# Kernel tuning notes

Hardware: AMD Instinct MI355X
Metric: run time of the kernel (lower is better)

## Reference

```python
import jax, jax.numpy as jnp
import numpy as np

D_MODEL = 1024
H = 16
D_K = D_MODEL // H
B = 4
S = 2048
NEG = -1.0e9


def setup_inputs() -> dict:
    key = jax.random.key(0)
    ks = jax.random.split(key, 12)
    scale = 1.0 / np.sqrt(D_MODEL)
    inp = {
        "q": jax.random.normal(ks[0], (B, S, D_MODEL), jnp.float32),
        "k": jax.random.normal(ks[1], (B, S, D_MODEL), jnp.float32),
        "v": jax.random.normal(ks[2], (B, S, D_MODEL), jnp.float32),
        "mask": jax.random.randint(ks[3], (1, 1, S, S), 0, 2, jnp.int32),
        # nn.Linear params: y = x @ W.T + b
        "Wq": jax.random.normal(ks[4], (D_MODEL, D_MODEL), jnp.float32) * scale,
        "bq": jnp.zeros((D_MODEL,), jnp.float32),
        "Wk": jax.random.normal(ks[5], (D_MODEL, D_MODEL), jnp.float32) * scale,
        "bk": jnp.zeros((D_MODEL,), jnp.float32),
        "Wv": jax.random.normal(ks[6], (D_MODEL, D_MODEL), jnp.float32) * scale,
        "bv": jnp.zeros((D_MODEL,), jnp.float32),
        "Wo": jax.random.normal(ks[7], (D_MODEL, D_MODEL), jnp.float32) * scale,
        "bo": jnp.zeros((D_MODEL,), jnp.float32),
    }
    return inp


def reference(q, k, v, mask, Wq, bq, Wk, bk, Wv, bv, Wo, bo):
    # QKV projections (torch Linear: x @ W.T + b)
    query = q @ Wq.T + bq                       # [B,S,D]
    key_ = k @ Wk.T + bk
    value = v @ Wv.T + bv
    # [B,S,D] -> [B,H,S,d_k]
    def split_heads(x):
        return x.reshape(B, S, H, D_K).transpose(0, 2, 1, 3)
    query, key_, value = split_heads(query), split_heads(key_), split_heads(value)
    # scaled dot-product attention
    scores = jnp.einsum("bhqd,bhkd->bhqk", query, key_) / np.sqrt(D_K)
    scores = jnp.where(mask == 0, NEG, scores)  # masked_fill(mask==0, -1e9)
    attn = jax.nn.softmax(scores, axis=-1)      # dropout p=0 -> identity
    x = jnp.einsum("bhqk,bhkd->bhqd", attn, value)
    # merge heads and output projection
    x = x.transpose(0, 2, 1, 3).reshape(B, S, D_MODEL)
    return x @ Wo.T + bo
```

## Files before the change

kernel.cpp:

```cpp
#include <hip/hip_runtime.h>
#include <hip/hip_bf16.h>

typedef __bf16 bf16;
typedef __bf16 bf16x8 __attribute__((ext_vector_type(8)));
typedef __bf16 bf16x4 __attribute__((ext_vector_type(4)));
typedef float  f32x4v __attribute__((ext_vector_type(4)));

#define MFMA16(a, b, c) __builtin_amdgcn_mfma_f32_16x16x32_bf16((a), (b), (c), 0, 0, 0)

static constexpr int D_MODEL = 1024;
static constexpr int NH      = 16;
static constexpr int DK      = 64;
static constexpr int BATCH   = 4;
static constexpr int SEQ     = 2048;

__device__ __forceinline__ void glds16(const void* g, void* l) {
    __builtin_amdgcn_global_load_lds((const __attribute__((address_space(1))) void*)g,
                                     (__attribute__((address_space(3))) void*)l, 16, 0, 0);
}

struct CvtArgs {
    const float* s[7];
    bf16* d[7];
    int n[7];
};

__global__ __launch_bounds__(256) void cvt7(CvtArgs a) {
    const int which = blockIdx.y;
    const int i = (blockIdx.x * 256 + threadIdx.x) * 8;
    if (i >= a.n[which]) return;
    const float4 v0 = *(const float4*)(a.s[which] + i);
    const float4 v1 = *(const float4*)(a.s[which] + i + 4);
    bf16x8 o = {(bf16)v0.x, (bf16)v0.y, (bf16)v0.z, (bf16)v0.w,
                (bf16)v1.x, (bf16)v1.y, (bf16)v1.z, (bf16)v1.w};
    *(bf16x8*)(a.d[which] + i) = o;
}

__global__ __launch_bounds__(256) void mask_prep(const int* __restrict__ m,
                                                 bf16* __restrict__ Mr) {
    const int o = blockIdx.x * 256 + threadIdx.x;
    const int row = o >> 11, j = o & 2047;
    const int g = j >> 6, idx = j & 63;
    const int incol = (g << 6) + (((idx >> 2) & 3) << 4) + ((idx >> 4) << 2) + (idx & 3);
    Mr[o] = m[row * 2048 + incol] ? (bf16)0.0f : (bf16)-16384.0f;
}

template <int MODE>
__global__ __launch_bounds__(256) void gemm_bt(const bf16* __restrict__ A,
                                               const bf16* __restrict__ W,
                                               const float* __restrict__ bias,
                                               void* __restrict__ outv) {
    __shared__ bf16 Als[128 * 32];
    __shared__ bf16 Bls[128 * 32];

    const int tid  = threadIdx.x;
    const int wave = tid >> 6;
    const int lane = tid & 63;
    const int l15  = lane & 15;
    const int quad = lane >> 4;
    const int L    = blockIdx.x;
    const int m0   = ((L & 7) | ((L >> 6) << 3)) * 128;
    const int n0   = ((L >> 3) & 7) * 128;
    const int wm   = (wave >> 1) * 64;
    const int wn   = (wave & 1) * 64;

    f32x4v acc[4][4];
#pragma unroll
    for (int i = 0; i < 4; ++i)
#pragma unroll
        for (int j = 0; j < 4; ++j) acc[i][j] = (f32x4v){0.f, 0.f, 0.f, 0.f};

    const int r_a    = wave * 16 + (lane >> 2);
    const int c_a    = (lane & 3) * 8;
    const int ldsoff = wave * 512;

    for (int k0 = 0; k0 < 1024; k0 += 32) {
        __syncthreads();
#pragma unroll
        for (int p = 0; p < 2; ++p) {
            const int row = p * 64 + r_a;
            glds16(A + (size_t)(m0 + row) * 1024 + k0 + c_a, &Als[p * 2048 + ldsoff]);
            glds16(W + (size_t)(n0 + row) * 1024 + k0 + c_a, &Bls[p * 2048 + ldsoff]);
        }
        __syncthreads();

        bf16x8 af[4], bfr[4];
#pragma unroll
        for (int i = 0; i < 4; ++i)
            af[i] = *(const bf16x8*)(&Als[(wm + i * 16 + l15) * 32 + quad * 8]);
#pragma unroll
        for (int j = 0; j < 4; ++j)
            bfr[j] = *(const bf16x8*)(&Bls[(wn + j * 16 + l15) * 32 + quad * 8]);
#pragma unroll
        for (int i = 0; i < 4; ++i)
#pragma unroll
            for (int j = 0; j < 4; ++j) acc[i][j] = MFMA16(af[i], bfr[j], acc[i][j]);
    }

#pragma unroll
    for (int j = 0; j < 4; ++j) {
        const int col = n0 + wn + j * 16 + l15;
        const float bs = bias[col];
        const int h = col >> 6, dk = col & 63;
        if (MODE == 1) {
            bf16* out = (bf16*)outv;
            const int sg = m0 + wm;
            const int bb = sg >> 11, sb = sg & 2047;
            const size_t rowbase = ((size_t)((bb * NH + h) * 64 + dk)) * SEQ + sb;
#pragma unroll
            for (int i = 0; i < 4; ++i) {
                bf16x4 v = {(bf16)(acc[i][j][0] + bs), (bf16)(acc[i][j][1] + bs),
                            (bf16)(acc[i][j][2] + bs), (bf16)(acc[i][j][3] + bs)};
                *(bf16x4*)(&out[rowbase + quad * 16 + i * 4]) = v;
            }
        } else {
#pragma unroll
            for (int i = 0; i < 4; ++i) {
                const int r4 = m0 + wm + i * 16 + quad * 4;
                const int b = r4 >> 11, sb = r4 & 2047;
                if (MODE == 2) {
                    float* out = (float*)outv;
#pragma unroll
                    for (int reg = 0; reg < 4; ++reg)
                        out[(size_t)(r4 + reg) * 1024 + col] = acc[i][j][reg] + bs;
                } else {
                    bf16* out = (bf16*)outv;
#pragma unroll
                    for (int reg = 0; reg < 4; ++reg)
                        out[((size_t)(b * NH + h) * SEQ + sb + reg) * 64 + dk] =
                            (bf16)(acc[i][j][reg] + bs);
                }
            }
        }
    }
}

__global__ __launch_bounds__(256, 2) void attn_kernel(const bf16* __restrict__ Qh,
                                                      const bf16* __restrict__ Kh,
                                                      const bf16* __restrict__ Vtg,
                                                      const bf16* __restrict__ Mr,
                                                      bf16* __restrict__ Xout) {
    __shared__ bf16 Kls[4096];
    __shared__ bf16 Vls[4096];

    const int tid  = threadIdx.x;
    const int wave = tid >> 6;
    const int lane = tid & 63;
    const int l15  = lane & 15;
    const int quad = lane >> 4;
    const int bh   = blockIdx.x;
    const int q0   = blockIdx.y * 256;

    const size_t base = (size_t)bh * SEQ * DK;
    const bf16* Q  = Qh + base;
    const bf16* K  = Kh + base;
    const bf16* Vg = Vtg + base;

    const int qw = q0 + wave * 64;
    bf16x8 aq[4][2];
#pragma unroll
    for (int rb = 0; rb < 4; ++rb)
#pragma unroll
        for (int kk = 0; kk < 2; ++kk)
            aq[rb][kk] = *(const bf16x8*)(Q + (size_t)(qw + rb * 16 + l15) * 64 +
                                          kk * 32 + quad * 8);

    bf16x8 ones;
#pragma unroll
    for (int t = 0; t < 8; ++t) ones[t] = (bf16)1.0f;

    f32x4v acc[4][4];
    f32x4v sacc[4];
#pragma unroll
    for (int rb = 0; rb < 4; ++rb) {
        sacc[rb] = (f32x4v){0.f, 0.f, 0.f, 0.f};
#pragma unroll
        for (int x = 0; x < 4; ++x) acc[rb][x] = (f32x4v){0.f, 0.f, 0.f, 0.f};
    }

    constexpr float CLOG = 0.125f * 1.4426950408889634f;
    const bf16* mbase = Mr + (size_t)(qw + l15) * 2048 + quad * 16;

    for (int kt = 0; kt < SEQ; kt += 64) {
        __syncthreads();
#pragma unroll
        for (int p = 0; p < 2; ++p) {
            const int kc = wave * 2 + p;
            glds16(K + (size_t)(kt + lane) * 64 + kc * 8, &Kls[kc * 512]);
            glds16(Vg + (size_t)lane * SEQ + kt + kc * 8, &Vls[kc * 512]);
        }
        bf16x8 mv[4][2];
#pragma unroll
        for (int rb = 0; rb < 4; ++rb)
#pragma unroll
            for (int h2 = 0; h2 < 2; ++h2)
                mv[rb][h2] = *(const bf16x8*)(mbase + (size_t)(rb * 16) * 2048 +
                                              kt + h2 * 8);
        __syncthreads();

        bf16x8 ak[4][2];
#pragma unroll
        for (int n16 = 0; n16 < 4; ++n16)
#pragma unroll
            for (int kk = 0; kk < 2; ++kk)
                ak[n16][kk] = *(const bf16x8*)(&Kls[((kk * 4 + quad) * 64 + n16 * 16 + l15) * 8]);

        bf16x8 pa[4][2];
#pragma unroll
        for (int rb = 0; rb < 4; ++rb) {
            f32x4v sv[4];
            __builtin_amdgcn_s_setprio(1);
#pragma unroll
            for (int n16 = 0; n16 < 4; ++n16) {
                f32x4v t = (f32x4v){0.f, 0.f, 0.f, 0.f};
                t = MFMA16(ak[n16][0], aq[rb][0], t);
                t = MFMA16(ak[n16][1], aq[rb][1], t);
                sv[n16] = t;
            }
            __builtin_amdgcn_s_setprio(0);
#pragma unroll
            for (int n16 = 0; n16 < 4; ++n16)
#pragma unroll
                for (int reg = 0; reg < 4; ++reg) {
                    const float e = exp2f(fmaf(sv[n16][reg], CLOG,
                                               (float)mv[rb][n16 >> 1][(n16 & 1) * 4 + reg]));
                    pa[rb][n16 >> 1][(n16 & 1) * 4 + reg] = (bf16)e;
                }
        }

        __builtin_amdgcn_s_setprio(1);
#pragma unroll
        for (int rb = 0; rb < 4; ++rb) {
            sacc[rb] = MFMA16(pa[rb][0], ones, sacc[rb]);
            sacc[rb] = MFMA16(pa[rb][1], ones, sacc[rb]);
        }
#pragma unroll
        for (int nt = 0; nt < 4; ++nt) {
            const bf16x8 bv0 = *(const bf16x8*)(&Vls[((quad * 2 + 0) * 64 + nt * 16 + l15) * 8]);
            const bf16x8 bv1 = *(const bf16x8*)(&Vls[((quad * 2 + 1) * 64 + nt * 16 + l15) * 8]);
#pragma unroll
            for (int rb = 0; rb < 4; ++rb) {
                acc[rb][nt] = MFMA16(pa[rb][0], bv0, acc[rb][nt]);
                acc[rb][nt] = MFMA16(pa[rb][1], bv1, acc[rb][nt]);
            }
        }
        __builtin_amdgcn_s_setprio(0);
    }

    const int b = bh >> 4, h = bh & 15;
#pragma unroll
    for (int rb = 0; rb < 4; ++rb) {
        float rinv[4];
#pragma unroll
        for (int reg = 0; reg < 4; ++reg) rinv[reg] = 1.0f / sacc[rb][reg];
#pragma unroll
        for (int nt = 0; nt < 4; ++nt)
#pragma unroll
            for (int reg = 0; reg < 4; ++reg) {
                const int sg = qw + rb * 16 + quad * 4 + reg;
                Xout[(size_t)(b * SEQ + sg) * D_MODEL + h * 64 + nt * 16 + l15] =
                    (bf16)(acc[rb][nt][reg] * rinv[reg]);
            }
    }
}

extern "C" void kernel_launch(void* const* d_in, const int* in_sizes, int n_in,
                              void* d_out, int out_size, void* d_ws, size_t ws_size,
                              hipStream_t stream) {
    const float* q    = (const float*)d_in[0];
    const float* k    = (const float*)d_in[1];
    const float* v    = (const float*)d_in[2];
    const int*   mask = (const int*)d_in[3];
    const float* Wq   = (const float*)d_in[4];
    const float* bq   = (const float*)d_in[5];
    const float* Wk   = (const float*)d_in[6];
    const float* bk   = (const float*)d_in[7];
    const float* Wv   = (const float*)d_in[8];
    const float* bv   = (const float*)d_in[9];
    const float* Wo   = (const float*)d_in[10];
    const float* bo   = (const float*)d_in[11];

    const size_t T = (size_t)BATCH * SEQ * D_MODEL;
    const size_t WN = (size_t)D_MODEL * D_MODEL;
    char* w = (char*)d_ws;
    bf16* Qh  = (bf16*)w;            w += T * 2;
    bf16* Kh  = (bf16*)w;            w += T * 2;
    bf16* Vt  = (bf16*)w;            w += T * 2;
    bf16* Mr  = (bf16*)w;            w += (size_t)SEQ * SEQ * 2;
    bf16* qb  = (bf16*)w;            w += T * 2;
    bf16* kb  = (bf16*)w;            w += T * 2;
    bf16* vb  = (bf16*)w;            w += T * 2;
    bf16* Wqb = (bf16*)w;            w += WN * 2;
    bf16* Wkb = (bf16*)w;            w += WN * 2;
    bf16* Wvb = (bf16*)w;            w += WN * 2;
    bf16* Wob = (bf16*)w;            w += WN * 2;

    CvtArgs ca;
    ca.s[0] = q;  ca.d[0] = qb;  ca.n[0] = (int)T;
    ca.s[1] = k;  ca.d[1] = kb;  ca.n[1] = (int)T;
    ca.s[2] = v;  ca.d[2] = vb;  ca.n[2] = (int)T;
    ca.s[3] = Wq; ca.d[3] = Wqb; ca.n[3] = (int)WN;
    ca.s[4] = Wk; ca.d[4] = Wkb; ca.n[4] = (int)WN;
    ca.s[5] = Wv; ca.d[5] = Wvb; ca.n[5] = (int)WN;
    ca.s[6] = Wo; ca.d[6] = Wob; ca.n[6] = (int)WN;

    cvt7<<<dim3(4096, 7), 256, 0, stream>>>(ca);
    mask_prep<<<dim3((SEQ * SEQ) / 256), 256, 0, stream>>>(mask, Mr);

    dim3 gg(512);
    gemm_bt<0><<<gg, 256, 0, stream>>>(qb, Wqb, bq, (void*)Qh);
    gemm_bt<0><<<gg, 256, 0, stream>>>(kb, Wkb, bk, (void*)Kh);
    gemm_bt<1><<<gg, 256, 0, stream>>>(vb, Wvb, bv, (void*)Vt);

    attn_kernel<<<dim3(BATCH * NH, SEQ / 256), 256, 0, stream>>>(Qh, Kh, Vt, Mr, qb);

    gemm_bt<2><<<gg, 256, 0, stream>>>(qb, Wob, bo, d_out);
}
```

Baseline: 391.7 us.

## Fuse prep launches, batch QKV GEMMs, double-buffer attention K/V, fold scale into Q

The mask preprocessing is merged into the conversion kernel, which now handles 8 elements per thread, and the three QKV projection GEMMs run as one launch with a 3D grid. The softmax scale is folded into the Q projection, and the mask bias seeds the score accumulator, so the exp path needs no fma. Attention K/V tiles are double-buffered in LDS, prefetching the next tile while the current one is computed, with one barrier per iteration. This cuts launch overhead and load-latency stalls, but doubles attention LDS use, which may affect occupancy at 2 blocks per CU.

New measurement: 395.0 us. Within noise of the previous version (+0.8%).

```diff
diff --git a/kernel.cpp b/kernel.cpp
--- a/kernel.cpp
+++ b/kernel.cpp
@@ -13,6 +13,7 @@
 static constexpr int DK      = 64;
 static constexpr int BATCH   = 4;
 static constexpr int SEQ     = 2048;
+static constexpr float CLOG  = 0.125f * 1.4426950408889634f;
 
 __device__ __forceinline__ void glds16(const void* g, void* l) {
     __builtin_amdgcn_global_load_lds((const __attribute__((address_space(1))) void*)g,
@@ -23,11 +24,28 @@
     const float* s[7];
     bf16* d[7];
     int n[7];
+    const int* mask;
+    bf16* Mr;
 };
 
-__global__ __launch_bounds__(256) void cvt7(CvtArgs a) {
+__global__ __launch_bounds__(256) void cvt8(CvtArgs a) {
     const int which = blockIdx.y;
     const int i = (blockIdx.x * 256 + threadIdx.x) * 8;
+    if (which == 7) {
+        if (i >= SEQ * SEQ) return;
+        const int row = i >> 11, j0 = i & 2047;
+        const int g = j0 >> 6;
+        bf16x8 o;
+#pragma unroll
+        for (int t = 0; t < 8; ++t) {
+            const int idx = (j0 + t) & 63;
+            const int incol =
+                (g << 6) + (((idx >> 2) & 3) << 4) + ((idx >> 4) << 2) + (idx & 3);
+            o[t] = a.mask[row * 2048 + incol] ? (bf16)0.0f : (bf16)-16384.0f;
+        }
+        *(bf16x8*)(a.Mr + i) = o;
+        return;
+    }
     if (i >= a.n[which]) return;
     const float4 v0 = *(const float4*)(a.s[which] + i);
     const float4 v1 = *(const float4*)(a.s[which] + i + 4);
@@ -36,22 +54,22 @@
     *(bf16x8*)(a.d[which] + i) = o;
 }
 
-__global__ __launch_bounds__(256) void mask_prep(const int* __restrict__ m,
-                                                 bf16* __restrict__ Mr) {
-    const int o = blockIdx.x * 256 + threadIdx.x;
-    const int row = o >> 11, j = o & 2047;
-    const int g = j >> 6, idx = j & 63;
-    const int incol = (g << 6) + (((idx >> 2) & 3) << 4) + ((idx >> 4) << 2) + (idx & 3);
-    Mr[o] = m[row * 2048 + incol] ? (bf16)0.0f : (bf16)-16384.0f;
-}
-
-template <int MODE>
-__global__ __launch_bounds__(256) void gemm_bt(const bf16* __restrict__ A,
-                                               const bf16* __restrict__ W,
-                                               const float* __restrict__ bias,
-                                               void* __restrict__ outv) {
+struct G3 {
+    const bf16* A[3];
+    const bf16* W[3];
+    const float* bias[3];
+    bf16* out[3];
+};
+
+__global__ __launch_bounds__(256) void gemm_qkv(G3 g) {
     __shared__ bf16 Als[128 * 32];
     __shared__ bf16 Bls[128 * 32];
+
+    const int which = blockIdx.y;
+    const bf16* __restrict__ A   = g.A[which];
+    const bf16* __restrict__ W   = g.W[which];
+    const float* __restrict__ bias = g.bias[which];
+    const float scale = (which == 0) ? CLOG : 1.0f;
 
     const int tid  = threadIdx.x;
     const int wave = tid >> 6;
@@ -97,40 +115,97 @@
             for (int j = 0; j < 4; ++j) acc[i][j] = MFMA16(af[i], bfr[j], acc[i][j]);
     }
 
+    bf16* out = g.out[which];
+#pragma unroll
+    for (int j = 0; j < 4; ++j) {
+        const int col = n0 + wn + j * 16 + l15;
+        const float bs_s = bias[col] * scale;
+        const int h = col >> 6, dk = col & 63;
+        if (which == 2) {
+            const int sg = m0 + wm;
+            const int bb = sg >> 11, sb = sg & 2047;
+            const size_t rowbase = ((size_t)((bb * NH + h) * 64 + dk)) * SEQ + sb;
+#pragma unroll
+            for (int i = 0; i < 4; ++i) {
+                bf16x4 v = {(bf16)(acc[i][j][0] + bs_s), (bf16)(acc[i][j][1] + bs_s),
+                            (bf16)(acc[i][j][2] + bs_s), (bf16)(acc[i][j][3] + bs_s)};
+                *(bf16x4*)(&out[rowbase + quad * 16 + i * 4]) = v;
+            }
+        } else {
+#pragma unroll
+            for (int i = 0; i < 4; ++i) {
+                const int r4 = m0 + wm + i * 16 + quad * 4;
+                const int b = r4 >> 11, sb = r4 & 2047;
+#pragma unroll
+                for (int reg = 0; reg < 4; ++reg)
+                    out[((size_t)(b * NH + h) * SEQ + sb + reg) * 64 + dk] =
+                        (bf16)fmaf(acc[i][j][reg], scale, bs_s);
+            }
+        }
+    }
+}
+
+__global__ __launch_bounds__(256) void gemm_o(const bf16* __restrict__ A,
+                                              const bf16* __restrict__ W,
+                                              const float* __restrict__ bias,
+                                              float* __restrict__ out) {
+    __shared__ bf16 Als[128 * 32];
+    __shared__ bf16 Bls[128 * 32];
+
+    const int tid  = threadIdx.x;
+    const int wave = tid >> 6;
+    const int lane = tid & 63;
+    const int l15  = lane & 15;
+    const int quad = lane >> 4;
+    const int L    = blockIdx.x;
+    const int m0   = ((L & 7) | ((L >> 6) << 3)) * 128;
+    const int n0   = ((L >> 3) & 7) * 128;
+    const int wm   = (wave >> 1) * 64;
+    const int wn   = (wave & 1) * 64;
+
+    f32x4v acc[4][4];
+#pragma unroll
+    for (int i = 0; i < 4; ++i)
+#pragma unroll
+        for (int j = 0; j < 4; ++j) acc[i][j] = (f32x4v){0.f, 0.f, 0.f, 0.f};
+
+    const int r_a    = wave * 16 + (lane >> 2);
+    const int c_a    = (lane & 3) * 8;
+    const int ldsoff = wave * 512;
+
+    for (int k0 = 0; k0 < 1024; k0 += 32) {
+        __syncthreads();
+#pragma unroll
+        for (int p = 0; p < 2; ++p) {
+            const int row = p * 64 + r_a;
+            glds16(A + (size_t)(m0 + row) * 1024 + k0 + c_a, &Als[p * 2048 + ldsoff]);
+            glds16(W + (size_t)(n0 + row) * 1024 + k0 + c_a, &Bls[p * 2048 + ldsoff]);
+        }
+        __syncthreads();
+
+        bf16x8 af[4], bfr[4];
+#pragma unroll
+        for (int i = 0; i < 4; ++i)
+            af[i] = *(const bf16x8*)(&Als[(wm + i * 16 + l15) * 32 + quad * 8]);
+#pragma unroll
+        for (int j = 0; j < 4; ++j)
+            bfr[j] = *(const bf16x8*)(&Bls[(wn + j * 16 + l15) * 32 + quad * 8]);
+#pragma unroll
+        for (int i = 0; i < 4; ++i)
+#pragma unroll
+            for (int j = 0; j < 4; ++j) acc[i][j] = MFMA16(af[i], bfr[j], acc[i][j]);
+    }
+
 #pragma unroll
     for (int j = 0; j < 4; ++j) {
         const int col = n0 + wn + j * 16 + l15;
         const float bs = bias[col];
-        const int h = col >> 6, dk = col & 63;
-        if (MODE == 1) {
-            bf16* out = (bf16*)outv;
-            const int sg = m0 + wm;
-            const int bb = sg >> 11, sb = sg & 2047;
-            const size_t rowbase = ((size_t)((bb * NH + h) * 64 + dk)) * SEQ + sb;
-#pragma unroll
-            for (int i = 0; i < 4; ++i) {
-                bf16x4 v = {(bf16)(acc[i][j][0] + bs), (bf16)(acc[i][j][1] + bs),
-                            (bf16)(acc[i][j][2] + bs), (bf16)(acc[i][j][3] + bs)};
-                *(bf16x4*)(&out[rowbase + quad * 16 + i * 4]) = v;
-            }
-        } else {
-#pragma unroll
-            for (int i = 0; i < 4; ++i) {
-                const int r4 = m0 + wm + i * 16 + quad * 4;
-                const int b = r4 >> 11, sb = r4 & 2047;
-                if (MODE == 2) {
-                    float* out = (float*)outv;
-#pragma unroll
-                    for (int reg = 0; reg < 4; ++reg)
-                        out[(size_t)(r4 + reg) * 1024 + col] = acc[i][j][reg] + bs;
-                } else {
-                    bf16* out = (bf16*)outv;
-#pragma unroll
-                    for (int reg = 0; reg < 4; ++reg)
-                        out[((size_t)(b * NH + h) * SEQ + sb + reg) * 64 + dk] =
-                            (bf16)(acc[i][j][reg] + bs);
-                }
-            }
+#pragma unroll
+        for (int i = 0; i < 4; ++i) {
+            const int r4 = m0 + wm + i * 16 + quad * 4;
+#pragma unroll
+            for (int reg = 0; reg < 4; ++reg)
+                out[(size_t)(r4 + reg) * 1024 + col] = acc[i][j][reg] + bs;
         }
     }
 }
@@ -140,8 +215,8 @@
                                                       const bf16* __restrict__ Vtg,
                                                       const bf16* __restrict__ Mr,
                                                       bf16* __restrict__ Xout) {
-    __shared__ bf16 Kls[4096];
-    __shared__ bf16 Vls[4096];
+    __shared__ bf16 Kls[2][4096];
+    __shared__ bf16 Vls[2][4096];
 
     const int tid  = threadIdx.x;
     const int wave = tid >> 6;
@@ -178,17 +253,24 @@
         for (int x = 0; x < 4; ++x) acc[rb][x] = (f32x4v){0.f, 0.f, 0.f, 0.f};
     }
 
-    constexpr float CLOG = 0.125f * 1.4426950408889634f;
     const bf16* mbase = Mr + (size_t)(qw + l15) * 2048 + quad * 16;
 
-    for (int kt = 0; kt < SEQ; kt += 64) {
-        __syncthreads();
+    auto STAGE = [&](int kts, int bsel) {
 #pragma unroll
         for (int p = 0; p < 2; ++p) {
             const int kc = wave * 2 + p;
-            glds16(K + (size_t)(kt + lane) * 64 + kc * 8, &Kls[kc * 512]);
-            glds16(Vg + (size_t)lane * SEQ + kt + kc * 8, &Vls[kc * 512]);
-        }
+            glds16(K + (size_t)(kts + lane) * 64 + kc * 8, &Kls[bsel][kc * 512]);
+            glds16(Vg + (size_t)lane * SEQ + kts + kc * 8, &Vls[bsel][kc * 512]);
+        }
+    };
+
+    STAGE(0, 0);
+    __syncthreads();
+
+    for (int kt = 0; kt < SEQ; kt += 64) {
+        const int cur = (kt >> 6) & 1;
+        if (kt + 64 < SEQ) STAGE(kt + 64, cur ^ 1);
+
         bf16x8 mv[4][2];
 #pragma unroll
         for (int rb = 0; rb < 4; ++rb)
@@ -196,34 +278,41 @@
             for (int h2 = 0; h2 < 2; ++h2)
                 mv[rb][h2] = *(const bf16x8*)(mbase + (size_t)(rb * 16) * 2048 +
                                               kt + h2 * 8);
-        __syncthreads();
+
+        const bf16* Kb = &Kls[cur][0];
+        const bf16* Vb = &Vls[cur][0];
 
         bf16x8 ak[4][2];
 #pragma unroll
         for (int n16 = 0; n16 < 4; ++n16)
 #pragma unroll
             for (int kk = 0; kk < 2; ++kk)
-                ak[n16][kk] = *(const bf16x8*)(&Kls[((kk * 4 + quad) * 64 + n16 * 16 + l15) * 8]);
+                ak[n16][kk] = *(const bf16x8*)(&Kb[((kk * 4 + quad) * 64 + n16 * 16 + l15) * 8]);
 
         bf16x8 pa[4][2];
 #pragma unroll
         for (int rb = 0; rb < 4; ++rb) {
             f32x4v sv[4];
+#pragma unroll
+            for (int n16 = 0; n16 < 4; ++n16) {
+                f32x4v s;
+#pragma unroll
+                for (int reg = 0; reg < 4; ++reg)
+                    s[reg] = (float)mv[rb][n16 >> 1][(n16 & 1) * 4 + reg];
+                sv[n16] = s;
+            }
             __builtin_amdgcn_s_setprio(1);
 #pragma unroll
             for (int n16 = 0; n16 < 4; ++n16) {
-                f32x4v t = (f32x4v){0.f, 0.f, 0.f, 0.f};
-                t = MFMA16(ak[n16][0], aq[rb][0], t);
-                t = MFMA16(ak[n16][1], aq[rb][1], t);
-                sv[n16] = t;
+                sv[n16] = MFMA16(ak[n16][0], aq[rb][0], sv[n16]);
+                sv[n16] = MFMA16(ak[n16][1], aq[rb][1], sv[n16]);
             }
             __builtin_amdgcn_s_setprio(0);
 #pragma unroll
             for (int n16 = 0; n16 < 4; ++n16)
 #pragma unroll
                 for (int reg = 0; reg < 4; ++reg) {
-                    const float e = exp2f(fmaf(sv[n16][reg], CLOG,
-                                               (float)mv[rb][n16 >> 1][(n16 & 1) * 4 + reg]));
+                    const float e = exp2f(sv[n16][reg]);
                     pa[rb][n16 >> 1][(n16 & 1) * 4 + reg] = (bf16)e;
                 }
         }
@@ -236,8 +325,8 @@
         }
 #pragma unroll
         for (int nt = 0; nt < 4; ++nt) {
-            const bf16x8 bv0 = *(const bf16x8*)(&Vls[((quad * 2 + 0) * 64 + nt * 16 + l15) * 8]);
-            const bf16x8 bv1 = *(const bf16x8*)(&Vls[((quad * 2 + 1) * 64 + nt * 16 + l15) * 8]);
+            const bf16x8 bv0 = *(const bf16x8*)(&Vb[((quad * 2 + 0) * 64 + nt * 16 + l15) * 8]);
+            const bf16x8 bv1 = *(const bf16x8*)(&Vb[((quad * 2 + 1) * 64 + nt * 16 + l15) * 8]);
 #pragma unroll
             for (int rb = 0; rb < 4; ++rb) {
                 acc[rb][nt] = MFMA16(pa[rb][0], bv0, acc[rb][nt]);
@@ -245,6 +334,8 @@
             }
         }
         __builtin_amdgcn_s_setprio(0);
+
+        __syncthreads();
     }
 
     const int b = bh >> 4, h = bh & 15;
@@ -303,16 +394,18 @@
     ca.s[4] = Wk; ca.d[4] = Wkb; ca.n[4] = (int)WN;
     ca.s[5] = Wv; ca.d[5] = Wvb; ca.n[5] = (int)WN;
     ca.s[6] = Wo; ca.d[6] = Wob; ca.n[6] = (int)WN;
-
-    cvt7<<<dim3(4096, 7), 256, 0, stream>>>(ca);
-    mask_prep<<<dim3((SEQ * SEQ) / 256), 256, 0, stream>>>(mask, Mr);
-
-    dim3 gg(512);
-    gemm_bt<0><<<gg, 256, 0, stream>>>(qb, Wqb, bq, (void*)Qh);
-    gemm_bt<0><<<gg, 256, 0, stream>>>(kb, Wkb, bk, (void*)Kh);
-    gemm_bt<1><<<gg, 256, 0, stream>>>(vb, Wvb, bv, (void*)Vt);
+    ca.mask = mask;
+    ca.Mr   = Mr;
+
+    cvt8<<<dim3(4096, 8), 256, 0, stream>>>(ca);
+
+    G3 g3;
+    g3.A[0] = qb;  g3.W[0] = Wqb; g3.bias[0] = bq; g3.out[0] = Qh;
+    g3.A[1] = kb;  g3.W[1] = Wkb; g3.bias[1] = bk; g3.out[1] = Kh;
+    g3.A[2] = vb;  g3.W[2] = Wvb; g3.bias[2] = bv; g3.out[2] = Vt;
+    gemm_qkv<<<dim3(512, 3), 256, 0, stream>>>(g3);
 
     attn_kernel<<<dim3(BATCH * NH, SEQ / 256), 256, 0, stream>>>(Qh, Kh, Vt, Mr, qb);
 
-    gemm_bt<2><<<gg, 256, 0, stream>>>(qb, Wob, bo, d_out);
-}
+    gemm_o<<<dim3(512), 256, 0, stream>>>(qb, Wob, bo, (float*)d_out);
+}
```
